# Performance work log

Measured on AMD Instinct MI355X. Metric: run time of the kernel, lower is better.

## Reference

```python
import jax, jax.numpy as jnp
import numpy as np


def force_fn(x):
    # Harmonic force F = -grad U, U(x) = 0.5 * ||x||^2 (Ornstein-Uhlenbeck).
    return -x


def setup_inputs() -> dict:
    key = jax.random.key(0)
    x0 = jax.random.normal(key, (100000, 3), dtype=jnp.float32)
    return {
        "x0": x0,
        "gamma": jnp.ones((1,), dtype=jnp.float32),
        "kT": jnp.ones((1,), dtype=jnp.float32),
        "dt": jnp.ones((1,), dtype=jnp.float32) * 0.01,
        "n_steps": 1000,
        "store_every": 10,
    }


def reference(x0, gamma, kT, dt, n_steps, store_every):
    # Overdamped Langevin: x_{t+1} = x_t + F(x_t)/gamma * dt + sqrt(2*kT*dt/gamma) * N(0, I)
    gamma_s = gamma.reshape(())
    kT_s = kT.reshape(())
    dt_s = dt.reshape(())
    noise_scale = jnp.sqrt(2.0 * kT_s * dt_s / gamma_s)

    n_chunks = n_steps // store_every  # trajectory stored every `store_every` steps
    keys = jax.random.split(jax.random.key(42), n_chunks * store_every)
    keys = keys.reshape((n_chunks, store_every))

    def step(x, k):
        noise = jax.random.normal(k, x.shape, x.dtype)
        x_new = x + force_fn(x) / gamma_s * dt_s + noise_scale * noise
        return x_new, None

    def chunk(x, ks):
        x, _ = jax.lax.scan(step, x, ks)
        return x, x  # carry and store the state after each chunk

    _, traj = jax.lax.scan(chunk, x0, keys)  # (n_chunks, N, 3)
    return jnp.concatenate([x0[None], traj], axis=0)  # (n_chunks + 1, N, 3)
```

## Files before the change

### kernel.cpp

```cpp
#include <hip/hip_runtime.h>


#define KCAP 1024

struct alignas(16) Rec { unsigned s, b, c, a; };
struct KTable { Rec r[KCAP]; };

constexpr unsigned crotl(unsigned v, int r) { return (v << r) | (v >> (32 - r)); }

constexpr KTable gen_keys() {
    KTable t{};
    for (unsigned j = 0; j < KCAP; ++j) {
        const unsigned k0 = 0u, k1 = 42u, ks2 = k0 ^ k1 ^ 0x1BD11BDAu;
        unsigned x0 = 0u + k0, x1 = j + k1;
        const int rots[20] = {13,15,26,6, 17,29,16,24, 13,15,26,6, 17,29,16,24, 13,15,26,6};
        int ri = 0;
        for (int blk = 0; blk < 5; ++blk) {
            for (int rr = 0; rr < 4; ++rr) { x0 += x1; x1 = crotl(x1, rots[ri++]); x1 ^= x0; }
            switch (blk) {
                case 0: x0 += k1;  x1 += ks2 + 1u; break;
                case 1: x0 += ks2; x1 += k0 + 2u;  break;
                case 2: x0 += k0;  x1 += k1 + 3u;  break;
                case 3: x0 += k1;  x1 += ks2 + 4u; break;
                case 4: x0 += ks2; x1 += k0 + 5u;  break;
            }
        }
        const unsigned b0 = x0, b1 = x1;
        t.r[j] = Rec{b0 + b1, b1, b0 ^ b1 ^ 0x1BD11BDAu, b0};
    }
    return t;
}

__constant__ KTable KTAB = gen_keys();

#if __has_builtin(__builtin_amdgcn_alignbit)
#define ROTL(x, r) __builtin_amdgcn_alignbit((x), (x), 32u - (r))
#define SPLICE(bits) __builtin_amdgcn_alignbit(0x7Fu, (bits), 9u)
#else
#define ROTL(x, r) __builtin_rotateleft32((x), (r))
#define SPLICE(bits) (((bits) >> 9) | 0x3f800000u)
#endif

struct Consts {
    float P0, P1, P2, P3, P4, P5, P6, P7, P8;
    float NLN2, M25, M3, LO;
};

__device__ __forceinline__ float poly_lo(float w, const Consts& cc) {
    float p = cc.P0;
    p = fmaf(p, w, cc.P1);
    p = fmaf(p, w, cc.P2);
    p = fmaf(p, w, cc.P3);
    p = fmaf(p, w, cc.P4);
    p = fmaf(p, w, cc.P5);
    p = fmaf(p, w, cc.P6);
    p = fmaf(p, w, cc.P7);
    p = fmaf(p, w, cc.P8);
    return p;
}
__device__ __forceinline__ float poly_hi(float s) {
    float p =       -0.000200214257f;
    p = fmaf(p, s,   0.000100950558f);
    p = fmaf(p, s,   0.00134934322f);
    p = fmaf(p, s,  -0.00367342844f);
    p = fmaf(p, s,   0.00573950773f);
    p = fmaf(p, s,  -0.0076224613f);
    p = fmaf(p, s,   0.00943887047f);
    p = fmaf(p, s,   1.00167406f);
    p = fmaf(p, s,   2.83297682f);
    return p;
}

__device__ __forceinline__ unsigned tf_bits(Rec k, unsigned t) {
    unsigned x0 = k.s + t;
    unsigned x1 = ROTL(k.b + t, 13) ^ x0;
#define RND(r) { x0 += x1; x1 = ROTL(x1, r) ^ x0; }
    RND(15) RND(26) RND(6)
    x0 += k.b; x1 += k.c + 1u;
    RND(17) RND(29) RND(16) RND(24)
    x0 += k.c; x1 += k.a + 2u;
    RND(13) RND(15) RND(26) RND(6)
    x0 += k.a; x1 += k.b + 3u;
    RND(17) RND(29) RND(16) RND(24)
    x0 += k.b; x1 += k.c + 4u;
    RND(13) RND(15) RND(26) RND(6)
    x0 += k.c; x1 += k.a + 5u;
#undef RND
    return x0 ^ x1;
}

__device__ __forceinline__ float normal_of_bits(unsigned bits, const Consts& cc) {
    float F = __uint_as_float(SPLICE(bits));
    float u = fmaf(F, 2.0f, cc.M3);
    u = fmaxf(u, cc.LO);
    float h = fmaf(-u, u, 1.0f);
    float l2 = __log2f(h);
    float p;
    if (__builtin_expect(__any(l2 <= -7.2134752f), 0)) {
        float w  = l2 * cc.NLN2;
        float p1 = poly_lo(w + cc.M25, cc);
        float p2 = poly_hi(sqrtf(w) + cc.M3);
        p = (l2 > -7.2134752f) ? p1 : p2;
    } else {
        p = poly_lo(fmaf(l2, cc.NLN2, cc.M25), cc);
    }
    return p * u;
}

__device__ __forceinline__ Rec make_key(unsigned j) {
    const unsigned k0 = 0u, k1 = 42u, ks2 = k0 ^ k1 ^ 0x1BD11BDAu;
    unsigned x0 = k0, x1 = j + k1;
#define RND(r) { x0 += x1; x1 = ROTL(x1, r) ^ x0; }
    RND(13) RND(15) RND(26) RND(6)
    x0 += k1;  x1 += ks2 + 1u;
    RND(17) RND(29) RND(16) RND(24)
    x0 += ks2; x1 += k0 + 2u;
    RND(13) RND(15) RND(26) RND(6)
    x0 += k0;  x1 += k1 + 3u;
    RND(17) RND(29) RND(16) RND(24)
    x0 += k1;  x1 += ks2 + 4u;
    RND(13) RND(15) RND(26) RND(6)
    x0 += ks2; x1 += k0 + 5u;
#undef RND
    Rec r; r.s = x0 + x1; r.b = x1; r.c = x0 ^ x1 ^ 0x1BD11BDAu; r.a = x0;
    return r;
}

__device__ __forceinline__ bool fast_ok(int se, int ns, int n_chunks) {
    return se == 10 && n_chunks > 0 && ns / 10 == n_chunks && 10 * n_chunks <= KCAP;
}

__global__ __launch_bounds__(256) void langevin_noise(
    const float* __restrict__ gamma_p, const float* __restrict__ kT_p,
    const float* __restrict__ dt_p, const int* __restrict__ nsteps_p,
    const int* __restrict__ store_p, float* __restrict__ out,
    int E, int n_chunks)
{
    if (!fast_ok(*store_p, *nsteps_p, n_chunks)) return;
    const unsigned e = blockIdx.x * 256 + threadIdx.x;
    if ((int)e >= E) return;

    const float g  = gamma_p[0];
    const float kT = kT_p[0];
    const float dt = dt_p[0];
    float scale2 = sqrtf(2.0f * kT * dt / g) * 1.41421356f;
    const float na = -(dt / g);
    const float a  = 1.0f + na;

    Consts cc{2.81022636e-08f,  3.43273939e-07f, -3.5233877e-06f,
             -4.39150654e-06f,  0.00021858087f,  -0.00125372503f,
             -0.00417768164f,   0.246640727f,     1.50140941f,
             -0.69314718f,     -2.5f,            -3.0f, -0.99999994f};
    asm("" : "+v"(cc.P0), "+v"(cc.P1), "+v"(cc.P2), "+v"(cc.P3), "+v"(cc.P4),
             "+v"(cc.P5), "+v"(cc.P6), "+v"(cc.P7), "+v"(cc.P8),
             "+v"(cc.NLN2), "+v"(cc.M25), "+v"(cc.M3), "+v"(cc.LO));

    float w[10];
    w[9] = scale2;
#pragma unroll
    for (int s = 8; s >= 0; --s) w[s] = w[s + 1] * a;

    const int c0 = 2 * blockIdx.y;
    const int c1 = c0 + 1;
    const bool has1 = (c1 < n_chunks);

    float S0 = 0.0f, S1 = 0.0f;
#pragma unroll
    for (int s = 0; s < 10; ++s) {
        float z0 = normal_of_bits(tf_bits(KTAB.r[c0 * 10 + s], e), cc);
        S0 = fmaf(w[s], z0, S0);
        if (has1) {
            float z1 = normal_of_bits(tf_bits(KTAB.r[c1 * 10 + s], e), cc);
            S1 = fmaf(w[s], z1, S1);
        }
    }
    out[(size_t)(c0 + 1) * (size_t)E + e] = S0;
    if (has1) out[(size_t)(c1 + 1) * (size_t)E + e] = S1;
}

__global__ __launch_bounds__(256) void langevin_scan(
    const float* __restrict__ x0p,
    const int* __restrict__ nsteps_p, const int* __restrict__ store_p,
    const float* __restrict__ gamma_p, const float* __restrict__ dt_p,
    float* __restrict__ out, int E, int n_chunks)
{
    if (!fast_ok(*store_p, *nsteps_p, n_chunks)) return;
    const unsigned e = blockIdx.x * 256 + threadIdx.x;
    if ((int)e >= E) return;

    const float na = -(dt_p[0] / gamma_p[0]);
    float x = x0p[e];
    out[e] = x;
    float* p = out + (size_t)E + e;
#pragma unroll 2
    for (int c = 0; c < n_chunks; ++c) {
        float S = *p;
#pragma unroll
        for (int s = 0; s < 10; ++s) x = fmaf(na, x, x);
        x += S;
        *p = x;
        p += (size_t)E;
    }
}

__global__ __launch_bounds__(256) void langevin_generic(
    const float* __restrict__ x0p,
    const float* __restrict__ gamma_p, const float* __restrict__ kT_p,
    const float* __restrict__ dt_p, const int* __restrict__ nsteps_p,
    const int* __restrict__ store_p, float* __restrict__ out,
    int E, int n_chunks)
{
    const int ns = *nsteps_p;
    const int se = *store_p;
    if (fast_ok(se, ns, n_chunks)) return;
    const unsigned t = blockIdx.x * 256 + threadIdx.x;
    if ((int)t >= E) return;

    const float g  = gamma_p[0];
    const float kT = kT_p[0];
    const float dt = dt_p[0];
    float scale2 = sqrtf(2.0f * kT * dt / g) * 1.41421356f;
    float na = -(dt / g);

    Consts cc{2.81022636e-08f,  3.43273939e-07f, -3.5233877e-06f,
             -4.39150654e-06f,  0.00021858087f,  -0.00125372503f,
             -0.00417768164f,   0.246640727f,     1.50140941f,
             -0.69314718f,     -2.5f,            -3.0f, -0.99999994f};
    asm("" : "+v"(cc.P0), "+v"(cc.P1), "+v"(cc.P2), "+v"(cc.P3), "+v"(cc.P4),
             "+v"(cc.P5), "+v"(cc.P6), "+v"(cc.P7), "+v"(cc.P8),
             "+v"(cc.NLN2), "+v"(cc.M25), "+v"(cc.M3), "+v"(cc.LO),
             "+v"(scale2), "+v"(na));

    float x = x0p[t];
    out[t] = x;
    int frame = 1, since = 0;
#pragma unroll 1
    for (int s = 0; s < ns; ++s) {
        Rec k = (s < KCAP) ? KTAB.r[s] : make_key((unsigned)s);
        float z = normal_of_bits(tf_bits(k, t), cc);
        x = fmaf(scale2, z, fmaf(na, x, x));
        if (++since == se) {
            since = 0;
            if (frame <= n_chunks)
                out[(size_t)frame * (size_t)E + t] = x;
            ++frame;
        }
    }
}

extern "C" void kernel_launch(void* const* d_in, const int* in_sizes, int n_in,
                              void* d_out, int out_size, void* d_ws, size_t ws_size,
                              hipStream_t stream) {
    const float* x0    = (const float*)d_in[0];
    const float* gam   = (const float*)d_in[1];
    const float* kT    = (const float*)d_in[2];
    const float* dt    = (const float*)d_in[3];
    const int*   nst   = (const int*)d_in[4];
    const int*   sev   = (const int*)d_in[5];
    float*       out   = (float*)d_out;

    const int E = in_sizes[0];
    const int eb = (E + 255) / 256;
    int n_chunks = (E > 0) ? (out_size / E - 1) : -1;
    if (n_chunks < 1 || (size_t)(n_chunks + 1) * (size_t)E != (size_t)out_size)
        n_chunks = -1;

    langevin_generic<<<eb, 256, 0, stream>>>(x0, gam, kT, dt, nst, sev, out, E, n_chunks);

    if (n_chunks >= 1) {
        dim3 g1(eb, (n_chunks + 1) / 2);
        langevin_noise<<<g1, 256, 0, stream>>>(gam, kT, dt, nst, sev, out, E, n_chunks);
        langevin_scan<<<eb, 256, 0, stream>>>(x0, nst, sev, gam, dt, out, E, n_chunks);
    }
}
```

Before: 658.0 us.

## Pair elements per thread and use packed f32 FMA for normal transform

The noise kernel now has each thread handle two elements (e and e+256) for a single chunk, in place of one element across two chunks. This lets the inverse-erf polynomial, the scaling and the weighted accumulation run as v_pk_fma_f32/v_pk_mul_f32 on two lanes, roughly halving the VALU issue count for that part. The grid is rearranged to one chunk per y-block with half as many x-blocks, and log2 now goes through the amdgcn builtin. Threefry hashing is still scalar per element, and the packed path adds register pressure and divergence in the rare slow branch.

New measurement: 643.0 us. 1.02x faster.

```diff
diff --git a/kernel.cpp b/kernel.cpp
--- a/kernel.cpp
+++ b/kernel.cpp
@@ -2,6 +2,8 @@
 
 
 #define KCAP 1024
+
+typedef float v2f __attribute__((ext_vector_type(2)));
 
 struct alignas(16) Rec { unsigned s, b, c, a; };
 struct KTable { Rec r[KCAP]; };
@@ -41,21 +43,53 @@
 #define SPLICE(bits) (((bits) >> 9) | 0x3f800000u)
 #endif
 
-struct Consts {
-    float P0, P1, P2, P3, P4, P5, P6, P7, P8;
-    float NLN2, M25, M3, LO;
-};
-
-__device__ __forceinline__ float poly_lo(float w, const Consts& cc) {
-    float p = cc.P0;
-    p = fmaf(p, w, cc.P1);
-    p = fmaf(p, w, cc.P2);
-    p = fmaf(p, w, cc.P3);
-    p = fmaf(p, w, cc.P4);
-    p = fmaf(p, w, cc.P5);
-    p = fmaf(p, w, cc.P6);
-    p = fmaf(p, w, cc.P7);
-    p = fmaf(p, w, cc.P8);
+__device__ __forceinline__ float dev_log2(float h) {
+#if __has_builtin(__builtin_amdgcn_logf)
+    return __builtin_amdgcn_logf(h);
+#else
+    return __log2f(h);
+#endif
+}
+
+__device__ __forceinline__ v2f pk_fma(v2f a, v2f b, v2f c) {
+    v2f d;
+    asm("v_pk_fma_f32 %0, %1, %2, %3" : "=v"(d) : "v"(a), "v"(b), "v"(c));
+    return d;
+}
+__device__ __forceinline__ v2f pk_mul(v2f a, v2f b) {
+    v2f d;
+    asm("v_pk_mul_f32 %0, %1, %2" : "=v"(d) : "v"(a), "v"(b));
+    return d;
+}
+
+__device__ __forceinline__ unsigned tf_bits(Rec k, unsigned t) {
+    unsigned x0 = k.s + t;
+    unsigned x1 = ROTL(k.b + t, 13) ^ x0;
+#define RND(r) { x0 += x1; x1 = ROTL(x1, r) ^ x0; }
+    RND(15) RND(26) RND(6)
+    x0 += k.b; x1 += k.c + 1u;
+    RND(17) RND(29) RND(16) RND(24)
+    x0 += k.c; x1 += k.a + 2u;
+    RND(13) RND(15) RND(26) RND(6)
+    x0 += k.a; x1 += k.b + 3u;
+    RND(17) RND(29) RND(16) RND(24)
+    x0 += k.b; x1 += k.c + 4u;
+    RND(13) RND(15) RND(26) RND(6)
+    x0 += k.c; x1 += k.a + 5u;
+#undef RND
+    return x0 ^ x1;
+}
+
+__device__ __forceinline__ float poly_lo_lit(float w) {
+    float p =        2.81022636e-08f;
+    p = fmaf(p, w,   3.43273939e-07f);
+    p = fmaf(p, w,  -3.5233877e-06f);
+    p = fmaf(p, w,  -4.39150654e-06f);
+    p = fmaf(p, w,   0.00021858087f);
+    p = fmaf(p, w,  -0.00125372503f);
+    p = fmaf(p, w,  -0.00417768164f);
+    p = fmaf(p, w,   0.246640727f);
+    p = fmaf(p, w,   1.50140941f);
     return p;
 }
 __device__ __forceinline__ float poly_hi(float s) {
@@ -70,39 +104,57 @@
     p = fmaf(p, s,   2.83297682f);
     return p;
 }
-
-__device__ __forceinline__ unsigned tf_bits(Rec k, unsigned t) {
-    unsigned x0 = k.s + t;
-    unsigned x1 = ROTL(k.b + t, 13) ^ x0;
-#define RND(r) { x0 += x1; x1 = ROTL(x1, r) ^ x0; }
-    RND(15) RND(26) RND(6)
-    x0 += k.b; x1 += k.c + 1u;
-    RND(17) RND(29) RND(16) RND(24)
-    x0 += k.c; x1 += k.a + 2u;
-    RND(13) RND(15) RND(26) RND(6)
-    x0 += k.a; x1 += k.b + 3u;
-    RND(17) RND(29) RND(16) RND(24)
-    x0 += k.b; x1 += k.c + 4u;
-    RND(13) RND(15) RND(26) RND(6)
-    x0 += k.c; x1 += k.a + 5u;
-#undef RND
-    return x0 ^ x1;
-}
-
-__device__ __forceinline__ float normal_of_bits(unsigned bits, const Consts& cc) {
+__device__ __forceinline__ float slow_p(float l2) {
+    float w = l2 * -0.69314718f;
+    if (l2 > -7.2134752f) return poly_lo_lit(w - 2.5f);
+    return poly_hi(sqrtf(w) - 3.0f);
+}
+
+struct PkC { v2f c2, cM3, cNLN2, cM25, P0, P1, P2, P3, P4, P5, P6, P7, P8; };
+
+__device__ __forceinline__ v2f normal2(unsigned bA, unsigned bB, const PkC& pc) {
+    v2f F;
+    F.x = __uint_as_float(SPLICE(bA));
+    F.y = __uint_as_float(SPLICE(bB));
+    v2f u = pk_fma(F, pc.c2, pc.cM3);
+    u.x = fmaxf(u.x, -0.99999994f);
+    u.y = fmaxf(u.y, -0.99999994f);
+    v2f h;
+    h.x = fmaf(-u.x, u.x, 1.0f);
+    h.y = fmaf(-u.y, u.y, 1.0f);
+    v2f l2;
+    l2.x = dev_log2(h.x);
+    l2.y = dev_log2(h.y);
+    v2f p;
+    if (__builtin_expect(__any(fminf(l2.x, l2.y) <= -7.2134752f), 0)) {
+        p.x = slow_p(l2.x);
+        p.y = slow_p(l2.y);
+    } else {
+        v2f ww = pk_fma(l2, pc.cNLN2, pc.cM25);
+        p = pc.P0;
+        p = pk_fma(p, ww, pc.P1);
+        p = pk_fma(p, ww, pc.P2);
+        p = pk_fma(p, ww, pc.P3);
+        p = pk_fma(p, ww, pc.P4);
+        p = pk_fma(p, ww, pc.P5);
+        p = pk_fma(p, ww, pc.P6);
+        p = pk_fma(p, ww, pc.P7);
+        p = pk_fma(p, ww, pc.P8);
+    }
+    return pk_mul(p, u);
+}
+
+__device__ __forceinline__ float normal_of_bits(unsigned bits) {
     float F = __uint_as_float(SPLICE(bits));
-    float u = fmaf(F, 2.0f, cc.M3);
-    u = fmaxf(u, cc.LO);
+    float u = fmaf(F, 2.0f, -3.0f);
+    u = fmaxf(u, -0.99999994f);
     float h = fmaf(-u, u, 1.0f);
-    float l2 = __log2f(h);
+    float l2 = dev_log2(h);
     float p;
     if (__builtin_expect(__any(l2 <= -7.2134752f), 0)) {
-        float w  = l2 * cc.NLN2;
-        float p1 = poly_lo(w + cc.M25, cc);
-        float p2 = poly_hi(sqrtf(w) + cc.M3);
-        p = (l2 > -7.2134752f) ? p1 : p2;
+        p = slow_p(l2);
     } else {
-        p = poly_lo(fmaf(l2, cc.NLN2, cc.M25), cc);
+        p = poly_lo_lit(fmaf(l2, -0.69314718f, -2.5f));
     }
     return p * u;
 }
@@ -137,45 +189,59 @@
     int E, int n_chunks)
 {
     if (!fast_ok(*store_p, *nsteps_p, n_chunks)) return;
-    const unsigned e = blockIdx.x * 256 + threadIdx.x;
+    const unsigned e  = blockIdx.x * 512 + threadIdx.x;
+    const unsigned e2 = e + 256;
     if ((int)e >= E) return;
+    const bool has2 = ((int)e2 < E);
 
     const float g  = gamma_p[0];
     const float kT = kT_p[0];
     const float dt = dt_p[0];
-    float scale2 = sqrtf(2.0f * kT * dt / g) * 1.41421356f;
+    const float scale2 = sqrtf(2.0f * kT * dt / g) * 1.41421356f;
     const float na = -(dt / g);
     const float a  = 1.0f + na;
-
-    Consts cc{2.81022636e-08f,  3.43273939e-07f, -3.5233877e-06f,
-             -4.39150654e-06f,  0.00021858087f,  -0.00125372503f,
-             -0.00417768164f,   0.246640727f,     1.50140941f,
-             -0.69314718f,     -2.5f,            -3.0f, -0.99999994f};
-    asm("" : "+v"(cc.P0), "+v"(cc.P1), "+v"(cc.P2), "+v"(cc.P3), "+v"(cc.P4),
-             "+v"(cc.P5), "+v"(cc.P6), "+v"(cc.P7), "+v"(cc.P8),
-             "+v"(cc.NLN2), "+v"(cc.M25), "+v"(cc.M3), "+v"(cc.LO));
 
     float w[10];
     w[9] = scale2;
 #pragma unroll
     for (int s = 8; s >= 0; --s) w[s] = w[s + 1] * a;
-
-    const int c0 = 2 * blockIdx.y;
-    const int c1 = c0 + 1;
-    const bool has1 = (c1 < n_chunks);
-
-    float S0 = 0.0f, S1 = 0.0f;
+    v2f wp[10];
+#pragma unroll
+    for (int s = 0; s < 10; ++s) wp[s] = (v2f){w[s], w[s]};
+
+    PkC pc;
+    pc.c2    = (v2f){ 2.0f, 2.0f };
+    pc.cM3   = (v2f){-3.0f, -3.0f};
+    pc.cNLN2 = (v2f){-0.69314718f, -0.69314718f};
+    pc.cM25  = (v2f){-2.5f, -2.5f};
+    pc.P0 = (v2f){ 2.81022636e-08f,  2.81022636e-08f};
+    pc.P1 = (v2f){ 3.43273939e-07f,  3.43273939e-07f};
+    pc.P2 = (v2f){-3.5233877e-06f,  -3.5233877e-06f};
+    pc.P3 = (v2f){-4.39150654e-06f, -4.39150654e-06f};
+    pc.P4 = (v2f){ 0.00021858087f,   0.00021858087f};
+    pc.P5 = (v2f){-0.00125372503f,  -0.00125372503f};
+    pc.P6 = (v2f){-0.00417768164f,  -0.00417768164f};
+    pc.P7 = (v2f){ 0.246640727f,     0.246640727f};
+    pc.P8 = (v2f){ 1.50140941f,      1.50140941f};
+    asm("" : "+v"(pc.c2), "+v"(pc.cM3), "+v"(pc.cNLN2), "+v"(pc.cM25),
+             "+v"(pc.P0), "+v"(pc.P1), "+v"(pc.P2), "+v"(pc.P3), "+v"(pc.P4),
+             "+v"(pc.P5), "+v"(pc.P6), "+v"(pc.P7), "+v"(pc.P8));
+
+    const int c = blockIdx.y;
+    const Rec* kr = &KTAB.r[c * 10];
+
+    v2f S = (v2f){0.0f, 0.0f};
 #pragma unroll
     for (int s = 0; s < 10; ++s) {
-        float z0 = normal_of_bits(tf_bits(KTAB.r[c0 * 10 + s], e), cc);
-        S0 = fmaf(w[s], z0, S0);
-        if (has1) {
-            float z1 = normal_of_bits(tf_bits(KTAB.r[c1 * 10 + s], e), cc);
-            S1 = fmaf(w[s], z1, S1);
-        }
-    }
-    out[(size_t)(c0 + 1) * (size_t)E + e] = S0;
-    if (has1) out[(size_t)(c1 + 1) * (size_t)E + e] = S1;
+        const Rec k = kr[s];
+        unsigned bA = tf_bits(k, e);
+        unsigned bB = tf_bits(k, e2);
+        v2f z = normal2(bA, bB, pc);
+        S = pk_fma(wp[s], z, S);
+    }
+    float* op = out + (size_t)(c + 1) * (size_t)E;
+    op[e] = S.x;
+    if (has2) op[e2] = S.y;
 }
 
 __global__ __launch_bounds__(256) void langevin_scan(
@@ -222,22 +288,13 @@
     float scale2 = sqrtf(2.0f * kT * dt / g) * 1.41421356f;
     float na = -(dt / g);
 
-    Consts cc{2.81022636e-08f,  3.43273939e-07f, -3.5233877e-06f,
-             -4.39150654e-06f,  0.00021858087f,  -0.00125372503f,
-             -0.00417768164f,   0.246640727f,     1.50140941f,
-             -0.69314718f,     -2.5f,            -3.0f, -0.99999994f};
-    asm("" : "+v"(cc.P0), "+v"(cc.P1), "+v"(cc.P2), "+v"(cc.P3), "+v"(cc.P4),
-             "+v"(cc.P5), "+v"(cc.P6), "+v"(cc.P7), "+v"(cc.P8),
-             "+v"(cc.NLN2), "+v"(cc.M25), "+v"(cc.M3), "+v"(cc.LO),
-             "+v"(scale2), "+v"(na));
-
     float x = x0p[t];
     out[t] = x;
     int frame = 1, since = 0;
 #pragma unroll 1
     for (int s = 0; s < ns; ++s) {
         Rec k = (s < KCAP) ? KTAB.r[s] : make_key((unsigned)s);
-        float z = normal_of_bits(tf_bits(k, t), cc);
+        float z = normal_of_bits(tf_bits(k, t));
         x = fmaf(scale2, z, fmaf(na, x, x));
         if (++since == se) {
             since = 0;
@@ -268,7 +325,7 @@
     langevin_generic<<<eb, 256, 0, stream>>>(x0, gam, kT, dt, nst, sev, out, E, n_chunks);
 
     if (n_chunks >= 1) {
-        dim3 g1(eb, (n_chunks + 1) / 2);
+        dim3 g1((E + 511) / 512, n_chunks);
         langevin_noise<<<g1, 256, 0, stream>>>(gam, kT, dt, nst, sev, out, E, n_chunks);
         langevin_scan<<<eb, 256, 0, stream>>>(x0, nst, sev, gam, dt, out, E, n_chunks);
     }
```
